# Optimization experiments

Measured on AMD Instinct MI355X. Metric: run time of the kernel, lower is better.

The kernel has to match this reference:

```python
import jax, jax.numpy as jnp
import numpy as np

P = 0.5  # top-p threshold per edge type (self.p[etype] = 0.5)


def setup_inputs() -> dict:
    key = jax.random.key(0)
    ks = jax.random.split(key, 8)
    N, K, D_IN, D_OUT, C = 50000, 32, 128, 64, 2
    return {
        "feat": jax.random.normal(ks[0], (N, D_IN), dtype=jnp.float32),
        "W_mlp": jax.random.normal(ks[1], (D_IN, C), dtype=jnp.float32) * 0.05,
        "b_mlp": jax.random.normal(ks[2], (C,), dtype=jnp.float32) * 0.05,
        "W_lin": jax.random.normal(ks[3], (D_IN, D_OUT), dtype=jnp.float32) * 0.05,
        "b_lin": jax.random.normal(ks[4], (D_OUT,), dtype=jnp.float32) * 0.05,
        "nbr0": jax.random.randint(ks[5], (N, K), 0, N, dtype=jnp.int32),
        "nbr1": jax.random.randint(ks[6], (N, K), 0, N, dtype=jnp.int32),
        "nbr2": jax.random.randint(ks[7], (N, K), 0, N, dtype=jnp.int32),
    }


def reference(feat, W_mlp, b_mlp, W_lin, b_lin, nbr0, nbr1, nbr2):
    # feat: [N, D]; nbr*: [N, K] src-node ids of in-edges per edge type.
    K = nbr0.shape[1]
    num_sel = int(np.ceil(K * P))  # ceil(in_degree * p), constant for regular graph

    # tanh(MLP(h)) computed once per node: [N, C]
    mlp_h = jnp.tanh(feat @ W_mlp + b_mlp)

    def aggregate(nbr):
        # per-edge L1 distance: d = ||tanh(MLP(h_src)) - tanh(MLP(h_dst))||_1  -> [N, K]
        d = jnp.sum(jnp.abs(mlp_h[nbr] - mlp_h[:, None, :]), axis=-1)
        # keep num_sel SMALLEST distances per dst node (argpartition in original)
        _, idx = jax.lax.top_k(-d, num_sel)          # [N, num_sel]
        sel = jnp.take_along_axis(nbr, idx, axis=1)  # [N, num_sel] selected src ids
        # copy_u('h') + mean aggregation, then activation (tanh)
        return jnp.tanh(jnp.mean(feat[sel], axis=1))  # [N, D]

    h_homo = (P * aggregate(nbr0) + P * aggregate(nbr1) + P * aggregate(nbr2)) + feat
    h_homo = jnp.tanh(h_homo)
    return h_homo @ W_lin + b_lin
```

## Files before the change

kernel.cpp:

```cpp
#include <hip/hip_runtime.h>
#include <hip/hip_fp16.h>

#define N_NODES 50000
#define K 32
#define NSEL 16
#define D 128
#define DOUT 64
#define NTILES (N_NODES / 16)

typedef __attribute__((ext_vector_type(8))) _Float16 half8;
typedef __attribute__((ext_vector_type(4))) float floatx4;
typedef __attribute__((ext_vector_type(2))) float floatx2;

__device__ __forceinline__ unsigned int pack_h2(float a, float b) {
  union { __half2 h; unsigned int u; } c;
  c.h = __floats2half2_rn(a, b);
  return c.u;
}
__device__ __forceinline__ float fast_tanh(float x) {
  float e = __expf(2.f * x);
  return 1.f - __fdividef(2.f, 1.f + e);
}

__global__ __launch_bounds__(256) void mlp_kernel(
    const float* __restrict__ feat, const float* __restrict__ Wm,
    const float* __restrict__ bm, float2* __restrict__ mlp2,
    unsigned char* __restrict__ feat8 ) {
  const int wid = (blockIdx.x * blockDim.x + threadIdx.x) >> 6;
  const int lane = threadIdx.x & 63;
  const int sub = lane & 31;
  const int n = wid * 2 + (lane >> 5);

  float4 f = *(const float4*)(feat + (size_t)n * D + sub * 4);
  float4 w01 = *(const float4*)(Wm + sub * 8);
  float4 w23 = *(const float4*)(Wm + sub * 8 + 4);
  float p0 = f.x * w01.x + f.y * w01.z + f.z * w23.x + f.w * w23.z;
  float p1 = f.x * w01.y + f.y * w01.w + f.z * w23.y + f.w * w23.w;
#pragma unroll
  for (int off = 16; off; off >>= 1) {
    p0 += __shfl_xor(p0, off);
    p1 += __shfl_xor(p1, off);
  }
  int pk8 = __builtin_amdgcn_cvt_pk_fp8_f32(f.x, f.y, 0, false);
  pk8 = __builtin_amdgcn_cvt_pk_fp8_f32(f.z, f.w, pk8, true);
  *(unsigned int*)(feat8 + ((size_t)n << 7) + (sub << 2)) = (unsigned int)pk8;
  if (sub == 0) {
    mlp2[n] = make_float2(tanhf(p0 + bm[0]), tanhf(p1 + bm[1]));
  }
}

__global__ __launch_bounds__(256) void care_kernel(
    const float* __restrict__ feat, const unsigned char* __restrict__ feat8,
    const float2* __restrict__ mlp2, const int* __restrict__ nbr0,
    const int* __restrict__ nbr1, const int* __restrict__ nbr2,
    unsigned int* __restrict__ hfw ) {
  const int lane = threadIdx.x & 63;
  const int sub = lane & 31;
  const int hbase = (lane & 32) << 2;
  const int wid = (blockIdx.x * blockDim.x + threadIdx.x) >> 6;
  const int n = wid * 2 + (lane >> 5);

  const float2 my = mlp2[n];
  float4 acc = *(const float4*)(feat + (size_t)n * D + sub * 4);

  const int src0 = nbr0[n * K + sub];
  const int src1 = nbr1[n * K + sub];
  const int src2 = nbr2[n * K + sub];
  const float2 mh0 = mlp2[src0];
  const float2 mh1 = mlp2[src1];
  const float2 mh2 = mlp2[src2];
  const float d0 = fabsf(mh0.x - my.x) + fabsf(mh0.y - my.y);
  const float d1 = fabsf(mh1.x - my.x) + fabsf(mh1.y - my.y);
  const float d2 = fabsf(mh2.x - my.x) + fabsf(mh2.y - my.y);

  const int b0 = __float_as_int(d0);
  const int b1 = __float_as_int(d1);
  const int b2 = __float_as_int(d2);
  const unsigned long long ki0 =
      ((unsigned long long)(unsigned)b0 << 32) | (unsigned)sub;
  const unsigned long long ki1 =
      ((unsigned long long)(unsigned)b1 << 32) | (unsigned)sub;
  const unsigned long long ki2 =
      ((unsigned long long)(unsigned)b2 << 32) | (unsigned)sub;
  int c0 = 0, c1 = 0, c2 = 0;
#pragma unroll
  for (int j = 0; j < K; ++j) {
    const int aj = hbase + 4 * j;
    const unsigned a0 = (unsigned)__builtin_amdgcn_ds_bpermute(aj, b0);
    const unsigned a1 = (unsigned)__builtin_amdgcn_ds_bpermute(aj, b1);
    const unsigned a2 = (unsigned)__builtin_amdgcn_ds_bpermute(aj, b2);
    c0 += (((unsigned long long)a0 << 32) | (unsigned)j) < ki0;
    c1 += (((unsigned long long)a1 << 32) | (unsigned)j) < ki1;
    c2 += (((unsigned long long)a2 << 32) | (unsigned)j) < ki2;
  }

  int p0 = __builtin_amdgcn_ds_permute(hbase + (c0 << 2), src0);
  int p1 = __builtin_amdgcn_ds_permute(hbase + (c1 << 2), src1);
  int p2 = __builtin_amdgcn_ds_permute(hbase + (c2 << 2), src2);

  const unsigned sub4 = (unsigned)sub << 2;
  floatx2 A00 = {0.f, 0.f}, A01 = {0.f, 0.f};
  floatx2 A10 = {0.f, 0.f}, A11 = {0.f, 0.f};
  floatx2 A20 = {0.f, 0.f}, A21 = {0.f, 0.f};
#pragma unroll
  for (int t = 0; t < NSEL; ++t) {
    const int at = hbase + 4 * t;
    int r0 = __builtin_amdgcn_ds_bpermute(at, p0);
    int r1 = __builtin_amdgcn_ds_bpermute(at, p1);
    int r2 = __builtin_amdgcn_ds_bpermute(at, p2);
    unsigned int w0 = *(const unsigned int*)(feat8 + (((unsigned)r0 << 7) | sub4));
    unsigned int w1 = *(const unsigned int*)(feat8 + (((unsigned)r1 << 7) | sub4));
    unsigned int w2 = *(const unsigned int*)(feat8 + (((unsigned)r2 << 7) | sub4));
    A00 += __builtin_amdgcn_cvt_pk_f32_fp8(w0, false);
    A01 += __builtin_amdgcn_cvt_pk_f32_fp8(w0, true);
    A10 += __builtin_amdgcn_cvt_pk_f32_fp8(w1, false);
    A11 += __builtin_amdgcn_cvt_pk_f32_fp8(w1, true);
    A20 += __builtin_amdgcn_cvt_pk_f32_fp8(w2, false);
    A21 += __builtin_amdgcn_cvt_pk_f32_fp8(w2, true);
  }
  acc.x += 0.5f * fast_tanh(A00.x * (1.f / NSEL));
  acc.y += 0.5f * fast_tanh(A00.y * (1.f / NSEL));
  acc.z += 0.5f * fast_tanh(A01.x * (1.f / NSEL));
  acc.w += 0.5f * fast_tanh(A01.y * (1.f / NSEL));
  acc.x += 0.5f * fast_tanh(A10.x * (1.f / NSEL));
  acc.y += 0.5f * fast_tanh(A10.y * (1.f / NSEL));
  acc.z += 0.5f * fast_tanh(A11.x * (1.f / NSEL));
  acc.w += 0.5f * fast_tanh(A11.y * (1.f / NSEL));
  acc.x += 0.5f * fast_tanh(A20.x * (1.f / NSEL));
  acc.y += 0.5f * fast_tanh(A20.y * (1.f / NSEL));
  acc.z += 0.5f * fast_tanh(A21.x * (1.f / NSEL));
  acc.w += 0.5f * fast_tanh(A21.y * (1.f / NSEL));

  acc.x = fast_tanh(acc.x);
  acc.y = fast_tanh(acc.y);
  acc.z = fast_tanh(acc.z);
  acc.w = fast_tanh(acc.w);
  uint2 p;
  p.x = pack_h2(acc.x, acc.y);
  p.y = pack_h2(acc.z, acc.w);
  *(uint2*)(hfw + n * (D / 2) + sub * 2) = p;
}

__global__ __launch_bounds__(256) void gemm_kernel(
    const unsigned int* __restrict__ hfw, const float* __restrict__ Wl,
    const float* __restrict__ bl, float* __restrict__ out) {
  __shared__ _Float16 sB[16 * 64 * 8];

  for (int w = threadIdx.x; w < 4096; w += blockDim.x) {
    int f = w >> 8, l = (w >> 2) & 63, j2 = w & 3;
    int kk = f >> 2, nt = f & 3;
    int k = kk * 32 + ((l >> 4) << 3) + 2 * j2;
    int nn = nt * 16 + (l & 15);
    ((unsigned int*)sB)[w] = pack_h2(Wl[k * DOUT + nn], Wl[(k + 1) * DOUT + nn]);
  }
  __syncthreads();

  const int lane = threadIdx.x & 63;
  const int tile = blockIdx.x * 4 + (threadIdx.x >> 6);
  if (tile >= NTILES) return;
  const int m0 = tile * 16;

  floatx4 acc[4];
#pragma unroll
  for (int nt = 0; nt < 4; ++nt) {
    float bn = bl[nt * 16 + (lane & 15)];
    acc[nt] = (floatx4){bn, bn, bn, bn};
  }
  const _Float16* hf = (const _Float16*)hfw;
#pragma unroll
  for (int kk = 0; kk < 4; ++kk) {
    half8 a = *(const half8*)(hf + (size_t)(m0 + (lane & 15)) * D + kk * 32 +
                              ((lane >> 4) << 3));
#pragma unroll
    for (int nt = 0; nt < 4; ++nt) {
      half8 bfr = *(const half8*)(sB + ((kk * 4 + nt) * 64 + lane) * 8);
      acc[nt] = __builtin_amdgcn_mfma_f32_16x16x32_f16(a, bfr, acc[nt], 0, 0, 0);
    }
  }
#pragma unroll
  for (int nt = 0; nt < 4; ++nt) {
#pragma unroll
    for (int r = 0; r < 4; ++r) {
      int m = m0 + ((lane >> 4) << 2) + r;
      out[(size_t)m * DOUT + nt * 16 + (lane & 15)] = acc[nt][r];
    }
  }
}

extern "C" void kernel_launch(void* const* d_in, const int* in_sizes, int n_in,
                              void* d_out, int out_size, void* d_ws,
                              size_t ws_size, hipStream_t stream) {
  const float* feat = (const float*)d_in[0];
  const float* Wm = (const float*)d_in[1];
  const float* bm = (const float*)d_in[2];
  const float* Wl = (const float*)d_in[3];
  const float* bl = (const float*)d_in[4];
  const int* nbr0 = (const int*)d_in[5];
  const int* nbr1 = (const int*)d_in[6];
  const int* nbr2 = (const int*)d_in[7];
  float* out = (float*)d_out;
  float2* mlp2 = (float2*)d_ws;
  unsigned char* feat8 = (unsigned char*)d_ws + (512 << 10);

  mlp_kernel<<<N_NODES / 8, 256, 0, stream>>>(feat, Wm, bm, mlp2, feat8);
  care_kernel<<<N_NODES / 8, 256, 0, stream>>>(feat, feat8, mlp2, nbr0, nbr1,
                                               nbr2, (unsigned int*)d_out);
  gemm_kernel<<<(NTILES + 3) / 4, 256, 0, stream>>>((const unsigned int*)d_out,
                                                    Wl, bl, out);
}
```

Before: 67.13 us.

## Fuse neighbor aggregation with output GEMM through shared memory

Merges the aggregation kernel and the output linear layer into one kernel. Each 512-thread block aggregates 16 nodes, writes the fp16 hidden rows to LDS and runs the MFMA GEMM from LDS, so the global round-trip of the hidden matrix and one launch go away. The fp16 weight packing moves into the MLP kernel, and the mean-then-tanh scaling is folded into a single exp argument. The cost is that every block reloads the 16KB packed weights and only 4 of 8 waves run the MFMA stage.

```diff
diff --git a/kernel.cpp b/kernel.cpp
--- a/kernel.cpp
+++ b/kernel.cpp
@@ -6,7 +6,6 @@
 #define NSEL 16
 #define D 128
 #define DOUT 64
-#define NTILES (N_NODES / 16)
 
 typedef __attribute__((ext_vector_type(8))) _Float16 half8;
 typedef __attribute__((ext_vector_type(4))) float floatx4;
@@ -17,15 +16,26 @@
   c.h = __floats2half2_rn(a, b);
   return c.u;
 }
+__device__ __forceinline__ half8 as_h8(uint4 u) {
+  union { uint4 u; half8 v; } c;
+  c.u = u;
+  return c.v;
+}
 __device__ __forceinline__ float fast_tanh(float x) {
   float e = __expf(2.f * x);
   return 1.f - __fdividef(2.f, 1.f + e);
 }
+__device__ __forceinline__ float agg_tanh(float s) {
+  float e = __expf(s * 0.125f);
+  return 1.f - __fdividef(2.f, 1.f + e);
+}
 
 __global__ __launch_bounds__(256) void mlp_kernel(
     const float* __restrict__ feat, const float* __restrict__ Wm,
-    const float* __restrict__ bm, float2* __restrict__ mlp2,
-    unsigned char* __restrict__ feat8 ) {
+    const float* __restrict__ bm, const float* __restrict__ Wl,
+    float2* __restrict__ mlp2,
+    unsigned char* __restrict__ feat8 ,
+    unsigned int* __restrict__ Whp ) {
   const int wid = (blockIdx.x * blockDim.x + threadIdx.x) >> 6;
   const int lane = threadIdx.x & 63;
   const int sub = lane & 31;
@@ -47,18 +57,36 @@
   if (sub == 0) {
     mlp2[n] = make_float2(tanhf(p0 + bm[0]), tanhf(p1 + bm[1]));
   }
-}
-
-__global__ __launch_bounds__(256) void care_kernel(
+  if (blockIdx.x < 16) {
+    const int wd = blockIdx.x * 256 + threadIdx.x;
+    const int fr = wd >> 8, l = (wd >> 2) & 63, j2 = wd & 3;
+    const int kk = fr >> 2, nt = fr & 3;
+    const int k = kk * 32 + ((l >> 4) << 3) + 2 * j2;
+    const int nn = nt * 16 + (l & 15);
+    Whp[wd] = pack_h2(Wl[k * DOUT + nn], Wl[(k + 1) * DOUT + nn]);
+  }
+}
+
+__global__ __launch_bounds__(512) void care_gemm_kernel(
     const float* __restrict__ feat, const unsigned char* __restrict__ feat8,
     const float2* __restrict__ mlp2, const int* __restrict__ nbr0,
     const int* __restrict__ nbr1, const int* __restrict__ nbr2,
-    unsigned int* __restrict__ hfw ) {
-  const int lane = threadIdx.x & 63;
+    const unsigned int* __restrict__ Whp, const float* __restrict__ bl,
+    float* __restrict__ out) {
+  __shared__ __align__(16) unsigned int sW[4096];
+  __shared__ __align__(16) unsigned int sH[16][68];
+
+  const int tid = threadIdx.x;
+#pragma unroll
+  for (int i = 0; i < 8; ++i) sW[tid + i * 512] = Whp[tid + i * 512];
+
+  const int lane = tid & 63;
   const int sub = lane & 31;
+  const int h = lane >> 5;
+  const int w = tid >> 6;
+  const int nl = w * 2 + h;
   const int hbase = (lane & 32) << 2;
-  const int wid = (blockIdx.x * blockDim.x + threadIdx.x) >> 6;
-  const int n = wid * 2 + (lane >> 5);
+  const int n = blockIdx.x * 16 + nl;
 
   const float2 my = mlp2[n];
   float4 acc = *(const float4*)(feat + (size_t)n * D + sub * 4);
@@ -98,7 +126,7 @@
   int p1 = __builtin_amdgcn_ds_permute(hbase + (c1 << 2), src1);
   int p2 = __builtin_amdgcn_ds_permute(hbase + (c2 << 2), src2);
 
-  const unsigned sub4 = (unsigned)sub << 2;
+  const unsigned char* f8o = feat8 + ((unsigned)sub << 2);
   floatx2 A00 = {0.f, 0.f}, A01 = {0.f, 0.f};
   floatx2 A10 = {0.f, 0.f}, A11 = {0.f, 0.f};
   floatx2 A20 = {0.f, 0.f}, A21 = {0.f, 0.f};
@@ -108,9 +136,9 @@
     int r0 = __builtin_amdgcn_ds_bpermute(at, p0);
     int r1 = __builtin_amdgcn_ds_bpermute(at, p1);
     int r2 = __builtin_amdgcn_ds_bpermute(at, p2);
-    unsigned int w0 = *(const unsigned int*)(feat8 + (((unsigned)r0 << 7) | sub4));
-    unsigned int w1 = *(const unsigned int*)(feat8 + (((unsigned)r1 << 7) | sub4));
-    unsigned int w2 = *(const unsigned int*)(feat8 + (((unsigned)r2 << 7) | sub4));
+    unsigned int w0 = *(const unsigned int*)(f8o + ((unsigned)r0 << 7));
+    unsigned int w1 = *(const unsigned int*)(f8o + ((unsigned)r1 << 7));
+    unsigned int w2 = *(const unsigned int*)(f8o + ((unsigned)r2 << 7));
     A00 += __builtin_amdgcn_cvt_pk_f32_fp8(w0, false);
     A01 += __builtin_amdgcn_cvt_pk_f32_fp8(w0, true);
     A10 += __builtin_amdgcn_cvt_pk_f32_fp8(w1, false);
@@ -118,71 +146,46 @@
     A20 += __builtin_amdgcn_cvt_pk_f32_fp8(w2, false);
     A21 += __builtin_amdgcn_cvt_pk_f32_fp8(w2, true);
   }
-  acc.x += 0.5f * fast_tanh(A00.x * (1.f / NSEL));
-  acc.y += 0.5f * fast_tanh(A00.y * (1.f / NSEL));
-  acc.z += 0.5f * fast_tanh(A01.x * (1.f / NSEL));
-  acc.w += 0.5f * fast_tanh(A01.y * (1.f / NSEL));
-  acc.x += 0.5f * fast_tanh(A10.x * (1.f / NSEL));
-  acc.y += 0.5f * fast_tanh(A10.y * (1.f / NSEL));
-  acc.z += 0.5f * fast_tanh(A11.x * (1.f / NSEL));
-  acc.w += 0.5f * fast_tanh(A11.y * (1.f / NSEL));
-  acc.x += 0.5f * fast_tanh(A20.x * (1.f / NSEL));
-  acc.y += 0.5f * fast_tanh(A20.y * (1.f / NSEL));
-  acc.z += 0.5f * fast_tanh(A21.x * (1.f / NSEL));
-  acc.w += 0.5f * fast_tanh(A21.y * (1.f / NSEL));
+  acc.x += 0.5f * agg_tanh(A00.x);
+  acc.y += 0.5f * agg_tanh(A00.y);
+  acc.z += 0.5f * agg_tanh(A01.x);
+  acc.w += 0.5f * agg_tanh(A01.y);
+  acc.x += 0.5f * agg_tanh(A10.x);
+  acc.y += 0.5f * agg_tanh(A10.y);
+  acc.z += 0.5f * agg_tanh(A11.x);
+  acc.w += 0.5f * agg_tanh(A11.y);
+  acc.x += 0.5f * agg_tanh(A20.x);
+  acc.y += 0.5f * agg_tanh(A20.y);
+  acc.z += 0.5f * agg_tanh(A21.x);
+  acc.w += 0.5f * agg_tanh(A21.y);
 
   acc.x = fast_tanh(acc.x);
   acc.y = fast_tanh(acc.y);
   acc.z = fast_tanh(acc.z);
   acc.w = fast_tanh(acc.w);
-  uint2 p;
-  p.x = pack_h2(acc.x, acc.y);
-  p.y = pack_h2(acc.z, acc.w);
-  *(uint2*)(hfw + n * (D / 2) + sub * 2) = p;
-}
-
-__global__ __launch_bounds__(256) void gemm_kernel(
-    const unsigned int* __restrict__ hfw, const float* __restrict__ Wl,
-    const float* __restrict__ bl, float* __restrict__ out) {
-  __shared__ _Float16 sB[16 * 64 * 8];
-
-  for (int w = threadIdx.x; w < 4096; w += blockDim.x) {
-    int f = w >> 8, l = (w >> 2) & 63, j2 = w & 3;
-    int kk = f >> 2, nt = f & 3;
-    int k = kk * 32 + ((l >> 4) << 3) + 2 * j2;
-    int nn = nt * 16 + (l & 15);
-    ((unsigned int*)sB)[w] = pack_h2(Wl[k * DOUT + nn], Wl[(k + 1) * DOUT + nn]);
-  }
+  uint2 hp;
+  hp.x = pack_h2(acc.x, acc.y);
+  hp.y = pack_h2(acc.z, acc.w);
+  *(uint2*)&sH[nl][sub * 2] = hp;
   __syncthreads();
 
-  const int lane = threadIdx.x & 63;
-  const int tile = blockIdx.x * 4 + (threadIdx.x >> 6);
-  if (tile >= NTILES) return;
-  const int m0 = tile * 16;
-
-  floatx4 acc[4];
-#pragma unroll
-  for (int nt = 0; nt < 4; ++nt) {
-    float bn = bl[nt * 16 + (lane & 15)];
-    acc[nt] = (floatx4){bn, bn, bn, bn};
-  }
-  const _Float16* hf = (const _Float16*)hfw;
-#pragma unroll
-  for (int kk = 0; kk < 4; ++kk) {
-    half8 a = *(const half8*)(hf + (size_t)(m0 + (lane & 15)) * D + kk * 32 +
-                              ((lane >> 4) << 3));
-#pragma unroll
-    for (int nt = 0; nt < 4; ++nt) {
-      half8 bfr = *(const half8*)(sB + ((kk * 4 + nt) * 64 + lane) * 8);
-      acc[nt] = __builtin_amdgcn_mfma_f32_16x16x32_f16(a, bfr, acc[nt], 0, 0, 0);
+  if (w < 4) {
+    const int nt = w;
+    const int m = lane & 15;
+    const int koff = (lane >> 4) * 4;
+    float bn = bl[nt * 16 + m];
+    floatx4 c4 = {bn, bn, bn, bn};
+#pragma unroll
+    for (int kk = 0; kk < 4; ++kk) {
+      uint4 aw = *(const uint4*)&sH[m][kk * 16 + koff];
+      uint4 bw = *(const uint4*)&sW[(kk * 4 + nt) * 256 + lane * 4];
+      c4 = __builtin_amdgcn_mfma_f32_16x16x32_f16(as_h8(aw), as_h8(bw), c4, 0,
+                                                  0, 0);
     }
-  }
-#pragma unroll
-  for (int nt = 0; nt < 4; ++nt) {
 #pragma unroll
     for (int r = 0; r < 4; ++r) {
-      int m = m0 + ((lane >> 4) << 2) + r;
-      out[(size_t)m * DOUT + nt * 16 + (lane & 15)] = acc[nt][r];
+      const int mr = ((lane >> 4) << 2) + r;
+      out[(size_t)(blockIdx.x * 16 + mr) * DOUT + nt * 16 + m] = c4[r];
     }
   }
 }
@@ -201,10 +204,11 @@
   float* out = (float*)d_out;
   float2* mlp2 = (float2*)d_ws;
   unsigned char* feat8 = (unsigned char*)d_ws + (512 << 10);
-
-  mlp_kernel<<<N_NODES / 8, 256, 0, stream>>>(feat, Wm, bm, mlp2, feat8);
-  care_kernel<<<N_NODES / 8, 256, 0, stream>>>(feat, feat8, mlp2, nbr0, nbr1,
-                                               nbr2, (unsigned int*)d_out);
-  gemm_kernel<<<(NTILES + 3) / 4, 256, 0, stream>>>((const unsigned int*)d_out,
-                                                    Wl, bl, out);
-}
+  unsigned int* Whp =
+      (unsigned int*)((char*)d_ws + (512 << 10) + (6400 << 10));
+
+  mlp_kernel<<<N_NODES / 8, 256, 0, stream>>>(feat, Wm, bm, Wl, mlp2, feat8,
+                                              Whp);
+  care_gemm_kernel<<<N_NODES / 16, 512, 0, stream>>>(
+      feat, feat8, mlp2, nbr0, nbr1, nbr2, Whp, bl, out);
+}
```

Measured after the change: 63.53 us. 5.4% less time.
